# Kernel tuning notes

Hardware: AMD Instinct MI355X
Metric: run time of the kernel (lower is better)

Reference implementation:

```python
import jax, jax.numpy as jnp
import numpy as np

D_MODEL = 2048
HEADS = 16


def setup_inputs() -> dict:
    key = jax.random.key(0)
    ks = jax.random.split(key, 9)
    s = 1.0 / np.sqrt(D_MODEL)
    x = jax.random.normal(ks[0], (2, 2048, D_MODEL), dtype=jnp.float32)
    wq = jax.random.uniform(ks[1], (D_MODEL, D_MODEL), jnp.float32, -s, s)
    wk = jax.random.uniform(ks[2], (D_MODEL, D_MODEL), jnp.float32, -s, s)
    wv = jax.random.uniform(ks[3], (D_MODEL, D_MODEL), jnp.float32, -s, s)
    wo = jax.random.uniform(ks[4], (D_MODEL, D_MODEL), jnp.float32, -s, s)
    bq = jax.random.uniform(ks[5], (D_MODEL,), jnp.float32, -s, s)
    bk = jax.random.uniform(ks[6], (D_MODEL,), jnp.float32, -s, s)
    bv = jax.random.uniform(ks[7], (D_MODEL,), jnp.float32, -s, s)
    bo = jax.random.uniform(ks[8], (D_MODEL,), jnp.float32, -s, s)
    return {"x": x, "wq": wq, "bq": bq, "wk": wk, "bk": bk,
            "wv": wv, "bv": bv, "wo": wo, "bo": bo}


def _split(t, heads):
    b, s, d = t.shape
    return t.reshape(b, s, heads, d // heads).transpose(0, 2, 1, 3)  # [b,h,s,dh]


def reference(x, wq, bq, wk, bk, wv, bv, wo, bo):
    q = x @ wq.T + bq
    k = x @ wk.T + bk
    v = x @ wv.T + bv
    q, k, v = _split(q, HEADS), _split(k, HEADS), _split(v, HEADS)
    dh = q.shape[-1]
    scale = 1.0 / np.sqrt(dh).astype(np.float32)
    score = jnp.einsum('bhqd,bhkd->bhqk', q, k) * scale  # [b,h,s,s]
    score = jax.nn.softmax(score.astype(jnp.float32), axis=-1).astype(q.dtype)
    out = jnp.einsum('bhqk,bhkd->bhqd', score, v)
    b, h, s, _ = out.shape
    out = out.transpose(0, 2, 1, 3).reshape(b, s, h * dh)
    return out @ wo.T + bo
```

## Files before the change

kernel.cpp:

```cpp
#include <hip/hip_runtime.h>
#include <cstdint>
#include <cstddef>

#define D_MODEL 2048
#define SEQ 2048
#define BATCH 2
#define HEADS 16
#define DH 128
#define MROWS (BATCH * SEQ)

typedef __attribute__((ext_vector_type(8))) short short8;
typedef __attribute__((ext_vector_type(4))) float f32x4;
typedef __attribute__((ext_vector_type(16))) float f32x16;
typedef __attribute__((ext_vector_type(2))) unsigned int uint2e;

__device__ __forceinline__ unsigned short f2bf(float f) {
    unsigned int u = __builtin_bit_cast(unsigned int, f);
    u += 0x7fffu + ((u >> 16) & 1u);
    return (unsigned short)(u >> 16);
}

__device__ __forceinline__ unsigned int cvt_pk_bf16(float lo, float hi) {
    unsigned int w;
    asm("v_cvt_pk_bf16_f32 %0, %1, %2" : "=v"(w) : "v"(lo), "v"(hi));
    return w;
}

__device__ __forceinline__ void swap32(unsigned int& x, unsigned int& y) {
#if __has_builtin(__builtin_amdgcn_permlane32_swap)
    uint2e r = __builtin_amdgcn_permlane32_swap(x, y, false, false);
    x = r[0]; y = r[1];
#else
    const int hi = (threadIdx.x >> 5) & 1;
    const unsigned int gx = (unsigned int)__shfl_xor((int)x, 32);
    const unsigned int gy = (unsigned int)__shfl_xor((int)y, 32);
    const unsigned int nx = hi ? gy : x;
    const unsigned int ny = hi ? y : gx;
    x = nx; y = ny;
#endif
}

__device__ __forceinline__ void gload_lds16(const unsigned short* g, unsigned short* l) {
    __builtin_amdgcn_global_load_lds(
        (const __attribute__((address_space(1))) void*)g,
        (__attribute__((address_space(3))) void*)l, 16, 0, 0);
}

__global__ __launch_bounds__(256) void cvt_kernel(const float* __restrict__ in,
                                                  unsigned short* __restrict__ out, int n4) {
    int i = blockIdx.x * 256 + threadIdx.x;
    if (i < n4) {
        const float4 v = reinterpret_cast<const float4*>(in)[i];
        ushort4 o;
        o.x = f2bf(v.x); o.y = f2bf(v.y); o.z = f2bf(v.z); o.w = f2bf(v.w);
        reinterpret_cast<ushort4*>(out)[i] = o;
    }
}

__global__ __launch_bounds__(256) void cvt4_kernel(const float* __restrict__ w0,
                                                   const float* __restrict__ w1,
                                                   const float* __restrict__ w2,
                                                   const float* __restrict__ w3,
                                                   unsigned short* __restrict__ out) {
    const int per = (D_MODEL * D_MODEL) / 4;
    int i = blockIdx.x * 256 + threadIdx.x;
    const int sel = i / per;
    const int off = i - sel * per;
    const float* s = sel == 0 ? w0 : sel == 1 ? w1 : sel == 2 ? w2 : w3;
    const float4 v = reinterpret_cast<const float4*>(s)[off];
    ushort4 o;
    o.x = f2bf(v.x); o.y = f2bf(v.y); o.z = f2bf(v.z); o.w = f2bf(v.w);
    reinterpret_cast<ushort4*>(out)[i] = o;
}

template <int MODE>
__global__ __launch_bounds__(512, 2)
void gemmT(const unsigned short* __restrict__ A,
           const unsigned short* __restrict__ W0,
           const unsigned short* __restrict__ W1,
           const unsigned short* __restrict__ W2,
           const float* __restrict__ b0f,
           const float* __restrict__ b1f,
           const float* __restrict__ b2f,
           unsigned short* __restrict__ O0,
           unsigned short* __restrict__ O1,
           unsigned short* __restrict__ O2,
           float* __restrict__ OF) {
    constexpr int BM = 256, BN = 128, BK = 64;
    constexpr int K = D_MODEL;
    constexpr int NTILES = K / BK;
    constexpr int NT_N = (MODE == 0 ? 48 : 16);
    constexpr int NWG = (MROWS / BM) * NT_N;
    constexpr int ASZ = BM * BK;
    constexpr int BSZ = BN * BK;
    __shared__ unsigned short As[3][ASZ];
    __shared__ unsigned short Bs[3][BSZ];

    const int tid  = threadIdx.x;
    const int lane = tid & 63;
    const int wid  = tid >> 6;

    const int wk = (blockIdx.x & 7) * (NWG >> 3) + (blockIdx.x >> 3);
    const int nt = wk % NT_N;
    const int mt = wk / NT_N;
    const int m0 = mt * BM;
    const int n0 = nt * BN;

    const unsigned short* Bw;
    const float* bias;
    int nloc;
    if constexpr (MODE == 0) {
        const int nsel = n0 >> 11;
        nloc = n0 & 2047;
        Bw = nsel == 0 ? W0 : (nsel == 1 ? W1 : W2);
        bias = nsel == 0 ? b0f : (nsel == 1 ? b1f : b2f);
    } else {
        Bw = W0; bias = b0f; nloc = n0;
    }

    const int srow = tid >> 3;
    const int sch  = tid & 7;
    const int ssw  = (sch ^ (srow & 7)) * 8;
    const int sd   = srow * 64 + sch * 8;
    const unsigned short* aS[4];
#pragma unroll
    for (int j = 0; j < 4; ++j) aS[j] = A + (size_t)(m0 + j * 64 + srow) * K + ssw;
    const unsigned short* bS[2];
#pragma unroll
    for (int j = 0; j < 2; ++j) bS[j] = Bw + (size_t)(nloc + j * 64 + srow) * K + ssw;

    const int fr = lane & 15, fg = lane >> 4;
    const int wm = wid >> 1, wn = wid & 1;
    int aoff[4][2], boff[4][2];
#pragma unroll
    for (int mi = 0; mi < 4; ++mi)
#pragma unroll
        for (int ks = 0; ks < 2; ++ks) {
            aoff[mi][ks] = (wm * 64 + mi * 16 + fr) * BK + ((ks * 4 + fg) ^ (fr & 7)) * 8;
            boff[mi][ks] = (wn * 64 + mi * 16 + fr) * BK + ((ks * 4 + fg) ^ (fr & 7)) * 8;
        }

    f32x4 acc[4][4] = {};

    unsigned short *pA0 = As[0], *pA1 = As[1], *pA2 = As[2];
    unsigned short *pB0 = Bs[0], *pB1 = Bs[1], *pB2 = Bs[2];

#define STG_A(P, T, J) gload_lds16(aS[J] + (T) * BK, (P) + (J) * 4096 + sd)
#define STG_B(P, T, J) gload_lds16(bS[J] + (T) * BK, (P) + (J) * 4096 + sd)

    STG_A(pA0, 0, 0); STG_A(pA0, 0, 1); STG_A(pA0, 0, 2); STG_A(pA0, 0, 3);
    STG_B(pB0, 0, 0); STG_B(pB0, 0, 1);
    STG_A(pA1, 1, 0); STG_A(pA1, 1, 1); STG_A(pA1, 1, 2); STG_A(pA1, 1, 3);
    STG_B(pB1, 1, 0); STG_B(pB1, 1, 1);
    asm volatile("s_waitcnt vmcnt(6)" ::: "memory");
    __builtin_amdgcn_s_barrier();

    for (int t = 0; t < NTILES; ++t) {
        const bool more = (t + 2 < NTILES);
        short8 aF[4][2], bF0[2][2];
#pragma unroll
        for (int mi = 0; mi < 4; ++mi)
#pragma unroll
            for (int ks = 0; ks < 2; ++ks)
                aF[mi][ks] = *(const short8*)&pA0[aoff[mi][ks]];
#pragma unroll
        for (int ni = 0; ni < 2; ++ni)
#pragma unroll
            for (int ks = 0; ks < 2; ++ks)
                bF0[ni][ks] = *(const short8*)&pB0[boff[ni][ks]];
        if (more) { STG_A(pA2, t + 2, 0); STG_A(pA2, t + 2, 1); STG_B(pB2, t + 2, 0); }
        __builtin_amdgcn_s_barrier();
        asm volatile("s_waitcnt lgkmcnt(0)" ::: "memory");
        __builtin_amdgcn_sched_barrier(0);
        __builtin_amdgcn_s_setprio(1);
#pragma unroll
        for (int ks = 0; ks < 2; ++ks)
#pragma unroll
            for (int mi = 0; mi < 4; ++mi)
#pragma unroll
                for (int ni = 0; ni < 2; ++ni)
                    acc[mi][ni] = __builtin_amdgcn_mfma_f32_16x16x32_bf16(
                        aF[mi][ks], bF0[ni][ks], acc[mi][ni], 0, 0, 0);
        __builtin_amdgcn_s_setprio(0);
        __builtin_amdgcn_s_barrier();
        short8 bF1[2][2];
#pragma unroll
        for (int ni = 0; ni < 2; ++ni)
#pragma unroll
            for (int ks = 0; ks < 2; ++ks)
                bF1[ni][ks] = *(const short8*)&pB0[boff[2 + ni][ks]];
        if (more) { STG_A(pA2, t + 2, 2); STG_A(pA2, t + 2, 3); STG_B(pB2, t + 2, 1); }
        __builtin_amdgcn_s_barrier();
        asm volatile("s_waitcnt lgkmcnt(0)" ::: "memory");
        __builtin_amdgcn_sched_barrier(0);
        __builtin_amdgcn_s_setprio(1);
#pragma unroll
        for (int ks = 0; ks < 2; ++ks)
#pragma unroll
            for (int mi = 0; mi < 4; ++mi)
#pragma unroll
                for (int ni = 0; ni < 2; ++ni)
                    acc[mi][2 + ni] = __builtin_amdgcn_mfma_f32_16x16x32_bf16(
                        aF[mi][ks], bF1[ni][ks], acc[mi][2 + ni], 0, 0, 0);
        __builtin_amdgcn_s_setprio(0);
        if (more) asm volatile("s_waitcnt vmcnt(6)" ::: "memory");
        else      asm volatile("s_waitcnt vmcnt(0)" ::: "memory");
        __builtin_amdgcn_s_barrier();
        unsigned short* tA = pA0; pA0 = pA1; pA1 = pA2; pA2 = tA;
        unsigned short* tB = pB0; pB0 = pB1; pB1 = pB2; pB2 = tB;
    }
#undef STG_A
#undef STG_B

    if constexpr (MODE == 0) {
        const int nsel = n0 >> 11;
        if (nsel == 2) {
#pragma unroll
            for (int mi = 0; mi < 4; ++mi)
#pragma unroll
                for (int ni = 0; ni < 4; ++ni) {
                    const int col = nloc + wn * 64 + ni * 16 + fr;
                    const int row0 = m0 + wm * 64 + mi * 16 + fg * 4;
                    const float bv = bias[col];
                    ushort4 o4;
                    o4.x = f2bf(acc[mi][ni][0] + bv);
                    o4.y = f2bf(acc[mi][ni][1] + bv);
                    o4.z = f2bf(acc[mi][ni][2] + bv);
                    o4.w = f2bf(acc[mi][ni][3] + bv);
                    *(ushort4*)&O2[(size_t)col * MROWS + row0] = o4;
                }
        } else {
            unsigned short* Co = nsel ? O1 : O0;
#pragma unroll
            for (int mi = 0; mi < 4; ++mi)
#pragma unroll
                for (int ni = 0; ni < 4; ++ni) {
                    const int col = nloc + wn * 64 + ni * 16 + fr;
                    const float bv = bias[col];
#pragma unroll
                    for (int r = 0; r < 4; ++r) {
                        const int row = m0 + wm * 64 + mi * 16 + fg * 4 + r;
                        Co[(size_t)row * D_MODEL + col] = f2bf(acc[mi][ni][r] + bv);
                    }
                }
        }
    } else {
#pragma unroll
        for (int mi = 0; mi < 4; ++mi)
#pragma unroll
            for (int ni = 0; ni < 4; ++ni) {
                const int col = nloc + wn * 64 + ni * 16 + fr;
                const float bv = bias[col];
#pragma unroll
                for (int r = 0; r < 4; ++r) {
                    const int row = m0 + wm * 64 + mi * 16 + fg * 4 + r;
                    OF[(size_t)row * D_MODEL + col] = acc[mi][ni][r] + bv;
                }
            }
    }
}

__global__ __launch_bounds__(256, 2)
void flash_attn3(const unsigned short* __restrict__ Q, const unsigned short* __restrict__ Kg,
                 const unsigned short* __restrict__ VT, unsigned short* __restrict__ O) {
    constexpr int KVB = 64;
    constexpr int NT = SEQ / KVB;
    __shared__ unsigned short Ks[2 * KVB * DH];
    __shared__ unsigned short Vs[2 * DH * KVB];

    const int tid  = threadIdx.x;
    const int lane = tid & 63;
    const int wid  = tid >> 6;
    const int l31  = lane & 31;
    const int hi   = lane >> 5;

    const int qt = blockIdx.x & 15;
    const int bh = blockIdx.x >> 4;
    const int b = bh >> 4, h = bh & 15;
    const int qrow = qt * 128 + wid * 32 + l31;

    const unsigned short* Qp = Q + ((size_t)b * SEQ + qrow) * D_MODEL + h * DH;
    const unsigned short* Kp = Kg + (size_t)b * SEQ * D_MODEL + h * DH;
    const unsigned short* Vp = VT + (size_t)(h * DH) * MROWS + (size_t)b * SEQ;

    short8 qf[8];
#pragma unroll
    for (int kk = 0; kk < 8; ++kk)
        qf[kk] = *(const short8*)(Qp + kk * 16 + hi * 8);

    f32x16 acc[4] = {};
    float m_run = -1e30f, l_run = 0.f;
    const float Cc = 0.088388347648318447f * 1.4426950408889634f;
    const float THR = 8.0f / Cc;

    int co[8];
#pragma unroll
    for (int kk = 0; kk < 8; ++kk) co[kk] = ((kk * 2 + hi) ^ (l31 & 7)) * 8;

    int kroff[4], vroff[4];
#pragma unroll
    for (int q = 0; q < 4; ++q) {
        const int row_l = wid * 16 + q * 4 + (lane >> 4);
        kroff[q] = row_l * D_MODEL + ((lane & 15) ^ (row_l & 7)) * 8;
        const int d_l = wid * 32 + q * 8 + (lane >> 3);
        vroff[q] = d_l * MROWS + ((lane & 7) ^ (d_l & 7)) * 8;
    }
    unsigned short* KsW = Ks + (wid * 16) * DH;
    unsigned short* VsW = Vs + (wid * 32) * KVB;

#pragma unroll
    for (int q = 0; q < 4; ++q) {
        gload_lds16(Kp + kroff[q], KsW + q * 4 * DH);
        gload_lds16(Vp + vroff[q], VsW + q * 8 * KVB);
    }
    __syncthreads();

    for (int t = 0; t < NT; ++t) {
        const int cur = t & 1;
        if (t + 1 < NT) {
            const unsigned short* Kt = Kp + (size_t)((t + 1) * KVB) * D_MODEL;
            const unsigned short* Vt = Vp + (t + 1) * KVB;
            unsigned short* kd = KsW + (cur ^ 1) * (KVB * DH);
            unsigned short* vd = VsW + (cur ^ 1) * (DH * KVB);
#pragma unroll
            for (int q = 0; q < 4; ++q) {
                gload_lds16(Kt + kroff[q], kd + q * 4 * DH);
                gload_lds16(Vt + vroff[q], vd + q * 8 * KVB);
            }
        }
        const unsigned short* Kc = Ks + cur * (KVB * DH);
        const unsigned short* Vc = Vs + cur * (DH * KVB);

        f32x16 st0 = {}, st1 = {};
        __builtin_amdgcn_s_setprio(1);
#pragma unroll
        for (int kk = 0; kk < 8; ++kk) {
            const short8 kf0 = *(const short8*)&Kc[l31 * DH + co[kk]];
            const short8 kf1 = *(const short8*)&Kc[(32 + l31) * DH + co[kk]];
            st0 = __builtin_amdgcn_mfma_f32_32x32x16_bf16(kf0, qf[kk], st0, 0, 0, 0);
            st1 = __builtin_amdgcn_mfma_f32_32x32x16_bf16(kf1, qf[kk], st1, 0, 0, 0);
        }
        __builtin_amdgcn_s_setprio(0);

        float lm = -1e30f;
#pragma unroll
        for (int r = 0; r < 16; ++r) lm = fmaxf(lm, fmaxf(st0[r], st1[r]));
        {
            unsigned int a = __builtin_bit_cast(unsigned int, lm), bb = a;
            swap32(a, bb);
            lm = fmaxf(lm, __builtin_bit_cast(float, hi ? a : bb));
        }
        if (__any(lm > m_run + THR)) {
            const float mn = fmaxf(m_run, lm);
            const float sf = __builtin_amdgcn_exp2f((m_run - mn) * Cc);
            m_run = mn;
            l_run *= sf;
#pragma unroll
            for (int db = 0; db < 4; ++db)
#pragma unroll
                for (int r = 0; r < 16; ++r) acc[db][r] *= sf;
        }
        const float mc = m_run * Cc;
        float p0[16], p1[16];
        float ps = 0.f;
#pragma unroll
        for (int r = 0; r < 16; ++r) {
            p0[r] = __builtin_amdgcn_exp2f(__builtin_fmaf(st0[r], Cc, -mc));
            p1[r] = __builtin_amdgcn_exp2f(__builtin_fmaf(st1[r], Cc, -mc));
            ps += p0[r] + p1[r];
        }
        {
            unsigned int a = __builtin_bit_cast(unsigned int, ps), bb = a;
            swap32(a, bb);
            ps += __builtin_bit_cast(float, hi ? a : bb);
        }
        l_run += ps;

        unsigned int W0[8], W1[8];
#pragma unroll
        for (int tt = 0; tt < 8; ++tt) {
            W0[tt] = cvt_pk_bf16(p0[2 * tt], p0[2 * tt + 1]);
            W1[tt] = cvt_pk_bf16(p1[2 * tt], p1[2 * tt + 1]);
        }
        swap32(W0[0], W0[2]); swap32(W0[1], W0[3]);
        swap32(W0[4], W0[6]); swap32(W0[5], W0[7]);
        swap32(W1[0], W1[2]); swap32(W1[1], W1[3]);
        swap32(W1[4], W1[6]); swap32(W1[5], W1[7]);
        short8 pf[4];
        {
            uint4 f;
            f.x = W0[0]; f.y = W0[1]; f.z = W0[2]; f.w = W0[3];
            pf[0] = __builtin_bit_cast(short8, f);
            f.x = W0[4]; f.y = W0[5]; f.z = W0[6]; f.w = W0[7];
            pf[1] = __builtin_bit_cast(short8, f);
            f.x = W1[0]; f.y = W1[1]; f.z = W1[2]; f.w = W1[3];
            pf[2] = __builtin_bit_cast(short8, f);
            f.x = W1[4]; f.y = W1[5]; f.z = W1[6]; f.w = W1[7];
            pf[3] = __builtin_bit_cast(short8, f);
        }

        __builtin_amdgcn_s_setprio(1);
#pragma unroll
        for (int db = 0; db < 4; ++db) {
#pragma unroll
            for (int kk16 = 0; kk16 < 4; ++kk16) {
                const short8 vf = *(const short8*)&Vc[(db * 32 + l31) * KVB + co[kk16]];
                acc[db] = __builtin_amdgcn_mfma_f32_32x32x16_bf16(vf, pf[kk16], acc[db], 0, 0, 0);
            }
        }
        __builtin_amdgcn_s_setprio(0);
        __syncthreads();
    }

    const float inv_l = 1.0f / l_run;
    unsigned short* Op = O + ((size_t)b * SEQ + qrow) * D_MODEL + h * DH;
#pragma unroll
    for (int db = 0; db < 4; ++db)
#pragma unroll
        for (int g = 0; g < 4; ++g) {
            ushort4 o4;
            o4.x = f2bf(acc[db][4 * g + 0] * inv_l);
            o4.y = f2bf(acc[db][4 * g + 1] * inv_l);
            o4.z = f2bf(acc[db][4 * g + 2] * inv_l);
            o4.w = f2bf(acc[db][4 * g + 3] * inv_l);
            *(ushort4*)(Op + db * 32 + g * 8 + hi * 4) = o4;
        }
}

extern "C" void kernel_launch(void* const* d_in, const int* in_sizes, int n_in,
                              void* d_out, int out_size, void* d_ws, size_t ws_size,
                              hipStream_t stream) {
    (void)in_sizes; (void)n_in; (void)out_size; (void)ws_size;
    const float* x  = (const float*)d_in[0];
    const float* wq = (const float*)d_in[1];
    const float* bq = (const float*)d_in[2];
    const float* wk = (const float*)d_in[3];
    const float* bk = (const float*)d_in[4];
    const float* wv = (const float*)d_in[5];
    const float* bv = (const float*)d_in[6];
    const float* wo = (const float*)d_in[7];
    const float* bo = (const float*)d_in[8];
    float* out = (float*)d_out;

    unsigned short* ws = (unsigned short*)d_ws;
    const size_t NX = (size_t)MROWS * D_MODEL;
    const size_t NW = (size_t)D_MODEL * D_MODEL;
    unsigned short* xb  = ws;
    unsigned short* wqb = xb + NX;
    unsigned short* wkb = wqb + NW;
    unsigned short* wvb = wkb + NW;
    unsigned short* wob = wvb + NW;
    unsigned short* Qb  = wob + NW;
    unsigned short* Kb  = Qb + NX;
    unsigned short* VTb = Kb + NX;
    unsigned short* Ab  = VTb + NX;

    cvt_kernel<<<(unsigned)(NX / 1024), 256, 0, stream>>>(x, xb, (int)(NX / 4));
    cvt4_kernel<<<(unsigned)(4 * NW / 1024), 256, 0, stream>>>(wq, wk, wv, wo, wqb);

    gemmT<0><<<768, 512, 0, stream>>>(xb, wqb, wkb, wvb, bq, bk, bv,
                                      Qb, Kb, VTb, nullptr);

    flash_attn3<<<512, 256, 0, stream>>>(Qb, Kb, VTb, Ab);

    gemmT<1><<<256, 512, 0, stream>>>(Ab, wob, nullptr, nullptr, bo, nullptr, nullptr,
                                      nullptr, nullptr, nullptr, out);
}
```

Baseline: 263.7 us.

## Shrink GEMM LDS pipeline to single A buffer and double B buffer for occupancy

```diff
diff --git a/kernel.cpp b/kernel.cpp
--- a/kernel.cpp
+++ b/kernel.cpp
@@ -74,8 +74,8 @@
 }
 
 template <int MODE>
-__global__ __launch_bounds__(512, 2)
-void gemmT(const unsigned short* __restrict__ A,
+__global__ __launch_bounds__(512, 4)
+void gemmS(const unsigned short* __restrict__ A,
            const unsigned short* __restrict__ W0,
            const unsigned short* __restrict__ W1,
            const unsigned short* __restrict__ W2,
@@ -91,10 +91,8 @@
     constexpr int NTILES = K / BK;
     constexpr int NT_N = (MODE == 0 ? 48 : 16);
     constexpr int NWG = (MROWS / BM) * NT_N;
-    constexpr int ASZ = BM * BK;
-    constexpr int BSZ = BN * BK;
-    __shared__ unsigned short As[3][ASZ];
-    __shared__ unsigned short Bs[3][BSZ];
+    __shared__ unsigned short As[BM * BK];
+    __shared__ unsigned short Bs[2][BN * BK];
 
     const int tid  = threadIdx.x;
     const int lane = tid & 63;
@@ -133,43 +131,48 @@
     const int wm = wid >> 1, wn = wid & 1;
     int aoff[4][2], boff[4][2];
 #pragma unroll
-    for (int mi = 0; mi < 4; ++mi)
+    for (int i = 0; i < 4; ++i)
 #pragma unroll
         for (int ks = 0; ks < 2; ++ks) {
-            aoff[mi][ks] = (wm * 64 + mi * 16 + fr) * BK + ((ks * 4 + fg) ^ (fr & 7)) * 8;
-            boff[mi][ks] = (wn * 64 + mi * 16 + fr) * BK + ((ks * 4 + fg) ^ (fr & 7)) * 8;
+            aoff[i][ks] = (wm * 64 + i * 16 + fr) * BK + ((ks * 4 + fg) ^ (fr & 7)) * 8;
+            boff[i][ks] = (wn * 64 + i * 16 + fr) * BK + ((ks * 4 + fg) ^ (fr & 7)) * 8;
         }
 
     f32x4 acc[4][4] = {};
 
-    unsigned short *pA0 = As[0], *pA1 = As[1], *pA2 = As[2];
-    unsigned short *pB0 = Bs[0], *pB1 = Bs[1], *pB2 = Bs[2];
-
-#define STG_A(P, T, J) gload_lds16(aS[J] + (T) * BK, (P) + (J) * 4096 + sd)
-#define STG_B(P, T, J) gload_lds16(bS[J] + (T) * BK, (P) + (J) * 4096 + sd)
-
-    STG_A(pA0, 0, 0); STG_A(pA0, 0, 1); STG_A(pA0, 0, 2); STG_A(pA0, 0, 3);
-    STG_B(pB0, 0, 0); STG_B(pB0, 0, 1);
-    STG_A(pA1, 1, 0); STG_A(pA1, 1, 1); STG_A(pA1, 1, 2); STG_A(pA1, 1, 3);
-    STG_B(pB1, 1, 0); STG_B(pB1, 1, 1);
-    asm volatile("s_waitcnt vmcnt(6)" ::: "memory");
+#define STG_A(T)                                                               \
+    {                                                                          \
+        _Pragma("unroll")                                                      \
+        for (int j = 0; j < 4; ++j)                                            \
+            gload_lds16(aS[j] + (T) * BK, As + j * 4096 + sd);                 \
+    }
+#define STG_B(T, BUF)                                                          \
+    {                                                                          \
+        _Pragma("unroll")                                                      \
+        for (int j = 0; j < 2; ++j)                                            \
+            gload_lds16(bS[j] + (T) * BK, Bs[BUF] + j * 4096 + sd);            \
+    }
+
+    STG_A(0)
+    STG_B(0, 0)
+    asm volatile("s_waitcnt vmcnt(0)" ::: "memory");
     __builtin_amdgcn_s_barrier();
 
     for (int t = 0; t < NTILES; ++t) {
-        const bool more = (t + 2 < NTILES);
-        short8 aF[4][2], bF0[2][2];
+        const int p = t & 1;
+        const bool more = (t + 1 < NTILES);
+        if (more) STG_B(t + 1, p ^ 1)
+        short8 aF[4][2], bF[2][2];
 #pragma unroll
         for (int mi = 0; mi < 4; ++mi)
 #pragma unroll
             for (int ks = 0; ks < 2; ++ks)
-                aF[mi][ks] = *(const short8*)&pA0[aoff[mi][ks]];
+                aF[mi][ks] = *(const short8*)&As[aoff[mi][ks]];
 #pragma unroll
         for (int ni = 0; ni < 2; ++ni)
 #pragma unroll
             for (int ks = 0; ks < 2; ++ks)
-                bF0[ni][ks] = *(const short8*)&pB0[boff[ni][ks]];
-        if (more) { STG_A(pA2, t + 2, 0); STG_A(pA2, t + 2, 1); STG_B(pB2, t + 2, 0); }
-        __builtin_amdgcn_s_barrier();
+                bF[ni][ks] = *(const short8*)&Bs[p][boff[ni][ks]];
         asm volatile("s_waitcnt lgkmcnt(0)" ::: "memory");
         __builtin_amdgcn_sched_barrier(0);
         __builtin_amdgcn_s_setprio(1);
@@ -180,17 +183,16 @@
 #pragma unroll
                 for (int ni = 0; ni < 2; ++ni)
                     acc[mi][ni] = __builtin_amdgcn_mfma_f32_16x16x32_bf16(
-                        aF[mi][ks], bF0[ni][ks], acc[mi][ni], 0, 0, 0);
+                        aF[mi][ks], bF[ni][ks], acc[mi][ni], 0, 0, 0);
         __builtin_amdgcn_s_setprio(0);
         __builtin_amdgcn_s_barrier();
-        short8 bF1[2][2];
+        if (more) STG_A(t + 1)
+        short8 bG[2][2];
 #pragma unroll
         for (int ni = 0; ni < 2; ++ni)
 #pragma unroll
             for (int ks = 0; ks < 2; ++ks)
-                bF1[ni][ks] = *(const short8*)&pB0[boff[2 + ni][ks]];
-        if (more) { STG_A(pA2, t + 2, 2); STG_A(pA2, t + 2, 3); STG_B(pB2, t + 2, 1); }
-        __builtin_amdgcn_s_barrier();
+                bG[ni][ks] = *(const short8*)&Bs[p][boff[2 + ni][ks]];
         asm volatile("s_waitcnt lgkmcnt(0)" ::: "memory");
         __builtin_amdgcn_sched_barrier(0);
         __builtin_amdgcn_s_setprio(1);
@@ -201,13 +203,10 @@
 #pragma unroll
                 for (int ni = 0; ni < 2; ++ni)
                     acc[mi][2 + ni] = __builtin_amdgcn_mfma_f32_16x16x32_bf16(
-                        aF[mi][ks], bF1[ni][ks], acc[mi][2 + ni], 0, 0, 0);
+                        aF[mi][ks], bG[ni][ks], acc[mi][2 + ni], 0, 0, 0);
         __builtin_amdgcn_s_setprio(0);
-        if (more) asm volatile("s_waitcnt vmcnt(6)" ::: "memory");
-        else      asm volatile("s_waitcnt vmcnt(0)" ::: "memory");
+        asm volatile("s_waitcnt vmcnt(0)" ::: "memory");
         __builtin_amdgcn_s_barrier();
-        unsigned short* tA = pA0; pA0 = pA1; pA1 = pA2; pA2 = tA;
-        unsigned short* tB = pB0; pB0 = pB1; pB1 = pB2; pB2 = tB;
     }
 #undef STG_A
 #undef STG_B
@@ -458,11 +457,11 @@
     cvt_kernel<<<(unsigned)(NX / 1024), 256, 0, stream>>>(x, xb, (int)(NX / 4));
     cvt4_kernel<<<(unsigned)(4 * NW / 1024), 256, 0, stream>>>(wq, wk, wv, wo, wqb);
 
-    gemmT<0><<<768, 512, 0, stream>>>(xb, wqb, wkb, wvb, bq, bk, bv,
+    gemmS<0><<<768, 512, 0, stream>>>(xb, wqb, wkb, wvb, bq, bk, bv,
                                       Qb, Kb, VTb, nullptr);
 
     flash_attn3<<<512, 256, 0, stream>>>(Qb, Kb, VTb, Ab);
 
-    gemmT<1><<<256, 512, 0, stream>>>(Ab, wob, nullptr, nullptr, bo, nullptr, nullptr,
+    gemmS<1><<<256, 512, 0, stream>>>(Ab, wob, nullptr, nullptr, bo, nullptr, nullptr,
                                       nullptr, nullptr, nullptr, out);
 }
```

New measurement: 288.2 us. 9.3% more time.

## Use 256x256 tiles with an 8-phase pipelined schedule for the QKV GEMM

Applied to the files above, without the earlier changes.

```diff
diff --git a/kernel.cpp b/kernel.cpp
--- a/kernel.cpp
+++ b/kernel.cpp
@@ -73,28 +73,184 @@
     reinterpret_cast<ushort4*>(out)[i] = o;
 }
 
+__global__ __launch_bounds__(512, 2)
+void gemm8p(const unsigned short* __restrict__ A,
+            const unsigned short* __restrict__ W0,
+            const unsigned short* __restrict__ W1,
+            const unsigned short* __restrict__ W2,
+            const float* __restrict__ b0f,
+            const float* __restrict__ b1f,
+            const float* __restrict__ b2f,
+            unsigned short* __restrict__ O0,
+            unsigned short* __restrict__ O1,
+            unsigned short* __restrict__ O2) {
+    constexpr int BK = 64;
+    constexpr int K = D_MODEL;
+    constexpr int NT_N = 24;
+    constexpr int NWG = 16 * NT_N;
+    __shared__ unsigned short As[2][16384];
+    __shared__ unsigned short Bs[2][16384];
+
+    const int tid  = threadIdx.x;
+    const int lane = tid & 63;
+    const int wid  = tid >> 6;
+
+    const int wk = (blockIdx.x & 7) * (NWG >> 3) + (blockIdx.x >> 3);
+    const int nt = wk % NT_N;
+    const int mt = wk / NT_N;
+    const int m0 = mt * 256;
+    const int nsel = nt >> 3;
+    const int nloc = (nt & 7) * 256;
+
+    const unsigned short* Bw = nsel == 0 ? W0 : (nsel == 1 ? W1 : W2);
+    const float* bias = nsel == 0 ? b0f : (nsel == 1 ? b1f : b2f);
+
+    const int srow = tid >> 3;
+    const int sch  = tid & 7;
+    const int ssw  = (sch ^ (srow & 7)) * 8;
+    const int sd   = srow * 64 + sch * 8;
+    const unsigned short* aS[4];
+    const unsigned short* bS[4];
+#pragma unroll
+    for (int j = 0; j < 4; ++j) {
+        aS[j] = A  + (size_t)(m0 + j * 64 + srow) * K + ssw;
+        bS[j] = Bw + (size_t)(nloc + j * 64 + srow) * K + ssw;
+    }
+
+    const int fr = lane & 15, fg = lane >> 4;
+    const int wm = wid >> 2, wn = wid & 3;
+    int aoffs[2], boffs[2];
+#pragma unroll
+    for (int ks = 0; ks < 2; ++ks) {
+        const int sw = ((ks * 4 + fg) ^ (fr & 7)) * 8;
+        aoffs[ks] = (wm * 128 + fr) * 64 + sw;
+        boffs[ks] = (wn * 64 + fr) * 64 + sw;
+    }
+
+    f32x4 acc[8][4] = {};
+
+#define STG_F(SET, T)                                                \
+    gload_lds16(aS[0] + (T) * BK, &As[SET][0 * 4096 + sd]);          \
+    gload_lds16(aS[1] + (T) * BK, &As[SET][1 * 4096 + sd]);          \
+    gload_lds16(bS[0] + (T) * BK, &Bs[SET][0 * 4096 + sd]);          \
+    gload_lds16(bS[1] + (T) * BK, &Bs[SET][1 * 4096 + sd]);
+#define STG_L(SET, T)                                                \
+    gload_lds16(aS[2] + (T) * BK, &As[SET][2 * 4096 + sd]);          \
+    gload_lds16(aS[3] + (T) * BK, &As[SET][3 * 4096 + sd]);          \
+    gload_lds16(bS[2] + (T) * BK, &Bs[SET][2 * 4096 + sd]);          \
+    gload_lds16(bS[3] + (T) * BK, &Bs[SET][3 * 4096 + sd]);
+#define RD_A(DST, SET, HB)                                           \
+    _Pragma("unroll") for (int mi = 0; mi < 4; ++mi)                 \
+    _Pragma("unroll") for (int ks = 0; ks < 2; ++ks)                 \
+        DST[mi][ks] = *(const short8*)&As[SET][(HB) + mi * 1024 + aoffs[ks]];
+#define RD_B(DST, SET, NB)                                           \
+    _Pragma("unroll") for (int ni = 0; ni < 2; ++ni)                 \
+    _Pragma("unroll") for (int ks = 0; ks < 2; ++ks)                 \
+        DST[ni][ks] = *(const short8*)&Bs[SET][((NB) + ni) * 1024 + boffs[ks]];
+#define PH_MFMA(AF, BF, MB, NB)                                      \
+    __builtin_amdgcn_s_barrier();                                    \
+    asm volatile("s_waitcnt lgkmcnt(0)" ::: "memory");               \
+    __builtin_amdgcn_sched_barrier(0);                               \
+    __builtin_amdgcn_s_setprio(1);                                   \
+    _Pragma("unroll") for (int ks = 0; ks < 2; ++ks)                 \
+    _Pragma("unroll") for (int mi = 0; mi < 4; ++mi)                 \
+    _Pragma("unroll") for (int ni = 0; ni < 2; ++ni)                 \
+        acc[(MB) + mi][(NB) + ni] = __builtin_amdgcn_mfma_f32_16x16x32_bf16( \
+            AF[mi][ks], BF[ni][ks], acc[(MB) + mi][(NB) + ni], 0, 0, 0);     \
+    __builtin_amdgcn_s_setprio(0);                                   \
+    __builtin_amdgcn_s_barrier();
+
+    STG_F(0, 0)
+    STG_L(0, 0)
+    STG_F(1, 1)
+    asm volatile("s_waitcnt vmcnt(4)" ::: "memory");
+    __builtin_amdgcn_s_barrier();
+
+#pragma unroll 1
+    for (int j = 0; j < 16; ++j) {
+        const int t0 = 2 * j;
+        const bool more = (j < 15);
+        short8 aF[4][2], aG[4][2], b01[2][2], b23[2][2];
+        RD_A(aF, 0, 0)
+        RD_B(b01, 0, 0)
+        STG_L(1, t0 + 1)
+        PH_MFMA(aF, b01, 0, 0)
+        RD_B(b23, 0, 2)
+        PH_MFMA(aF, b23, 0, 2)
+        RD_A(aG, 0, 4096)
+        PH_MFMA(aG, b23, 4, 2)
+        if (more) {
+            STG_F(0, t0 + 2)
+            asm volatile("s_waitcnt vmcnt(4)" ::: "memory");
+        } else {
+            asm volatile("s_waitcnt vmcnt(0)" ::: "memory");
+        }
+        PH_MFMA(aG, b01, 4, 0)
+        RD_A(aF, 1, 0)
+        RD_B(b01, 1, 0)
+        if (more) { STG_L(0, t0 + 2) }
+        PH_MFMA(aF, b01, 0, 0)
+        RD_B(b23, 1, 2)
+        PH_MFMA(aF, b23, 0, 2)
+        RD_A(aG, 1, 4096)
+        PH_MFMA(aG, b23, 4, 2)
+        if (more) {
+            STG_F(1, t0 + 3)
+            asm volatile("s_waitcnt vmcnt(4)" ::: "memory");
+        }
+        PH_MFMA(aG, b01, 4, 0)
+    }
+#undef STG_F
+#undef STG_L
+#undef RD_A
+#undef RD_B
+#undef PH_MFMA
+
+    if (nsel == 2) {
+#pragma unroll
+        for (int mi = 0; mi < 8; ++mi)
+#pragma unroll
+            for (int ni = 0; ni < 4; ++ni) {
+                const int col = nloc + wn * 64 + ni * 16 + fr;
+                const int row0 = m0 + wm * 128 + mi * 16 + fg * 4;
+                const float bv = bias[col];
+                ushort4 o4;
+                o4.x = f2bf(acc[mi][ni][0] + bv);
+                o4.y = f2bf(acc[mi][ni][1] + bv);
+                o4.z = f2bf(acc[mi][ni][2] + bv);
+                o4.w = f2bf(acc[mi][ni][3] + bv);
+                *(ushort4*)&O2[(size_t)col * MROWS + row0] = o4;
+            }
+    } else {
+        unsigned short* Co = nsel ? O1 : O0;
+#pragma unroll
+        for (int mi = 0; mi < 8; ++mi)
+#pragma unroll
+            for (int ni = 0; ni < 4; ++ni) {
+                const int col = nloc + wn * 64 + ni * 16 + fr;
+                const float bv = bias[col];
+#pragma unroll
+                for (int r = 0; r < 4; ++r) {
+                    const int row = m0 + wm * 128 + mi * 16 + fg * 4 + r;
+                    Co[(size_t)row * D_MODEL + col] = f2bf(acc[mi][ni][r] + bv);
+                }
+            }
+    }
+}
+
 template <int MODE>
 __global__ __launch_bounds__(512, 2)
 void gemmT(const unsigned short* __restrict__ A,
            const unsigned short* __restrict__ W0,
-           const unsigned short* __restrict__ W1,
-           const unsigned short* __restrict__ W2,
            const float* __restrict__ b0f,
-           const float* __restrict__ b1f,
-           const float* __restrict__ b2f,
-           unsigned short* __restrict__ O0,
-           unsigned short* __restrict__ O1,
-           unsigned short* __restrict__ O2,
            float* __restrict__ OF) {
     constexpr int BM = 256, BN = 128, BK = 64;
     constexpr int K = D_MODEL;
     constexpr int NTILES = K / BK;
-    constexpr int NT_N = (MODE == 0 ? 48 : 16);
+    constexpr int NT_N = 16;
     constexpr int NWG = (MROWS / BM) * NT_N;
-    constexpr int ASZ = BM * BK;
-    constexpr int BSZ = BN * BK;
-    __shared__ unsigned short As[3][ASZ];
-    __shared__ unsigned short Bs[3][BSZ];
+    __shared__ unsigned short As[3][BM * BK];
+    __shared__ unsigned short Bs[3][BN * BK];
 
     const int tid  = threadIdx.x;
     const int lane = tid & 63;
@@ -106,17 +262,9 @@
     const int m0 = mt * BM;
     const int n0 = nt * BN;
 
-    const unsigned short* Bw;
-    const float* bias;
-    int nloc;
-    if constexpr (MODE == 0) {
-        const int nsel = n0 >> 11;
-        nloc = n0 & 2047;
-        Bw = nsel == 0 ? W0 : (nsel == 1 ? W1 : W2);
-        bias = nsel == 0 ? b0f : (nsel == 1 ? b1f : b2f);
-    } else {
-        Bw = W0; bias = b0f; nloc = n0;
-    }
+    const unsigned short* Bw = W0;
+    const float* bias = b0f;
+    const int nloc = n0;
 
     const int srow = tid >> 3;
     const int sch  = tid & 7;
@@ -145,16 +293,17 @@
     unsigned short *pA0 = As[0], *pA1 = As[1], *pA2 = As[2];
     unsigned short *pB0 = Bs[0], *pB1 = Bs[1], *pB2 = Bs[2];
 
-#define STG_A(P, T, J) gload_lds16(aS[J] + (T) * BK, (P) + (J) * 4096 + sd)
-#define STG_B(P, T, J) gload_lds16(bS[J] + (T) * BK, (P) + (J) * 4096 + sd)
-
-    STG_A(pA0, 0, 0); STG_A(pA0, 0, 1); STG_A(pA0, 0, 2); STG_A(pA0, 0, 3);
-    STG_B(pB0, 0, 0); STG_B(pB0, 0, 1);
-    STG_A(pA1, 1, 0); STG_A(pA1, 1, 1); STG_A(pA1, 1, 2); STG_A(pA1, 1, 3);
-    STG_B(pB1, 1, 0); STG_B(pB1, 1, 1);
+#define STG_A3(P, T) { _Pragma("unroll") for (int j = 0; j < 4; ++j) \
+        gload_lds16(aS[j] + (T) * BK, (P) + j * 4096 + sd); }
+#define STG_B3(P, T) { _Pragma("unroll") for (int j = 0; j < 2; ++j) \
+        gload_lds16(bS[j] + (T) * BK, (P) + j * 4096 + sd); }
+
+    STG_A3(pA0, 0) STG_B3(pB0, 0)
+    STG_A3(pA1, 1) STG_B3(pB1, 1)
     asm volatile("s_waitcnt vmcnt(6)" ::: "memory");
     __builtin_amdgcn_s_barrier();
 
+#pragma unroll 1
     for (int t = 0; t < NTILES; ++t) {
         const bool more = (t + 2 < NTILES);
         short8 aF[4][2], bF0[2][2];
@@ -168,8 +317,7 @@
 #pragma unroll
             for (int ks = 0; ks < 2; ++ks)
                 bF0[ni][ks] = *(const short8*)&pB0[boff[ni][ks]];
-        if (more) { STG_A(pA2, t + 2, 0); STG_A(pA2, t + 2, 1); STG_B(pB2, t + 2, 0); }
-        __builtin_amdgcn_s_barrier();
+        if (more) { STG_A3(pA2, t + 2) STG_B3(pB2, t + 2) }
         asm volatile("s_waitcnt lgkmcnt(0)" ::: "memory");
         __builtin_amdgcn_sched_barrier(0);
         __builtin_amdgcn_s_setprio(1);
@@ -182,15 +330,12 @@
                     acc[mi][ni] = __builtin_amdgcn_mfma_f32_16x16x32_bf16(
                         aF[mi][ks], bF0[ni][ks], acc[mi][ni], 0, 0, 0);
         __builtin_amdgcn_s_setprio(0);
-        __builtin_amdgcn_s_barrier();
-        short8 bF1[2][2];
+        short8 bG[2][2];
 #pragma unroll
         for (int ni = 0; ni < 2; ++ni)
 #pragma unroll
             for (int ks = 0; ks < 2; ++ks)
-                bF1[ni][ks] = *(const short8*)&pB0[boff[2 + ni][ks]];
-        if (more) { STG_A(pA2, t + 2, 2); STG_A(pA2, t + 2, 3); STG_B(pB2, t + 2, 1); }
-        __builtin_amdgcn_s_barrier();
+                bG[ni][ks] = *(const short8*)&pB0[boff[2 + ni][ks]];
         asm volatile("s_waitcnt lgkmcnt(0)" ::: "memory");
         __builtin_amdgcn_sched_barrier(0);
         __builtin_amdgcn_s_setprio(1);
@@ -201,7 +346,7 @@
 #pragma unroll
                 for (int ni = 0; ni < 2; ++ni)
                     acc[mi][2 + ni] = __builtin_amdgcn_mfma_f32_16x16x32_bf16(
-                        aF[mi][ks], bF1[ni][ks], acc[mi][2 + ni], 0, 0, 0);
+                        aF[mi][ks], bG[ni][ks], acc[mi][2 + ni], 0, 0, 0);
         __builtin_amdgcn_s_setprio(0);
         if (more) asm volatile("s_waitcnt vmcnt(6)" ::: "memory");
         else      asm volatile("s_waitcnt vmcnt(0)" ::: "memory");
@@ -209,55 +354,21 @@
         unsigned short* tA = pA0; pA0 = pA1; pA1 = pA2; pA2 = tA;
         unsigned short* tB = pB0; pB0 = pB1; pB1 = pB2; pB2 = tB;
     }
-#undef STG_A
-#undef STG_B
-
-    if constexpr (MODE == 0) {
-        const int nsel = n0 >> 11;
-        if (nsel == 2) {
-#pragma unroll
-            for (int mi = 0; mi < 4; ++mi)
-#pragma unroll
-                for (int ni = 0; ni < 4; ++ni) {
-                    const int col = nloc + wn * 64 + ni * 16 + fr;
-                    const int row0 = m0 + wm * 64 + mi * 16 + fg * 4;
-                    const float bv = bias[col];
-                    ushort4 o4;
-                    o4.x = f2bf(acc[mi][ni][0] + bv);
-                    o4.y = f2bf(acc[mi][ni][1] + bv);
-                    o4.z = f2bf(acc[mi][ni][2] + bv);
-                    o4.w = f2bf(acc[mi][ni][3] + bv);
-                    *(ushort4*)&O2[(size_t)col * MROWS + row0] = o4;
-                }
-        } else {
-            unsigned short* Co = nsel ? O1 : O0;
-#pragma unroll
-            for (int mi = 0; mi < 4; ++mi)
-#pragma unroll
-                for (int ni = 0; ni < 4; ++ni) {
-                    const int col = nloc + wn * 64 + ni * 16 + fr;
-                    const float bv = bias[col];
-#pragma unroll
-                    for (int r = 0; r < 4; ++r) {
-                        const int row = m0 + wm * 64 + mi * 16 + fg * 4 + r;
-                        Co[(size_t)row * D_MODEL + col] = f2bf(acc[mi][ni][r] + bv);
-                    }
-                }
-        }
-    } else {
-#pragma unroll
-        for (int mi = 0; mi < 4; ++mi)
-#pragma unroll
-            for (int ni = 0; ni < 4; ++ni) {
-                const int col = nloc + wn * 64 + ni * 16 + fr;
-                const float bv = bias[col];
-#pragma unroll
-                for (int r = 0; r < 4; ++r) {
-                    const int row = m0 + wm * 64 + mi * 16 + fg * 4 + r;
-                    OF[(size_t)row * D_MODEL + col] = acc[mi][ni][r] + bv;
-                }
+#undef STG_A3
+#undef STG_B3
+
+#pragma unroll
+    for (int mi = 0; mi < 4; ++mi)
+#pragma unroll
+        for (int ni = 0; ni < 4; ++ni) {
+            const int col = nloc + wn * 64 + ni * 16 + fr;
+            const float bv = bias[col];
+#pragma unroll
+            for (int r = 0; r < 4; ++r) {
+                const int row = m0 + wm * 64 + mi * 16 + fg * 4 + r;
+                OF[(size_t)row * D_MODEL + col] = acc[mi][ni][r] + bv;
             }
-    }
+        }
 }
 
 __global__ __launch_bounds__(256, 2)
@@ -458,11 +569,9 @@
     cvt_kernel<<<(unsigned)(NX / 1024), 256, 0, stream>>>(x, xb, (int)(NX / 4));
     cvt4_kernel<<<(unsigned)(4 * NW / 1024), 256, 0, stream>>>(wq, wk, wv, wo, wqb);
 
-    gemmT<0><<<768, 512, 0, stream>>>(xb, wqb, wkb, wvb, bq, bk, bv,
-                                      Qb, Kb, VTb, nullptr);
+    gemm8p<<<384, 512, 0, stream>>>(xb, wqb, wkb, wvb, bq, bk, bv, Qb, Kb, VTb);
 
     flash_attn3<<<512, 256, 0, stream>>>(Qb, Kb, VTb, Ab);
 
-    gemmT<1><<<256, 512, 0, stream>>>(Ab, wob, nullptr, nullptr, bo, nullptr, nullptr,
-                                      nullptr, nullptr, nullptr, out);
-}
+    gemmT<1><<<256, 512, 0, stream>>>(Ab, wob, bo, out);
+}
```

Result: slower. 275.2 us (+4.4%).
